# Kernel optimization log

Measured on AMD Instinct MI355X. Metric: run time of the kernel, lower is better.

## Reference

```python
import jax, jax.numpy as jnp
import numpy as np

B, S, D = 4, 2048, 1024  # batch, steps, d_model
HEAD, DIM = 16, 64       # head*dim == D


def setup_inputs() -> dict:
    key = jax.random.key(0)
    ks = jax.random.split(key, 7)
    mk = lambda k, shp, scale: (jax.random.normal(k, shp, dtype=jnp.float32) * scale)
    w_scale = np.sqrt(2.0 / D).astype(np.float32)  # he_normal-ish
    return {
        "query": mk(ks[0], (B, S, D), 1.0),
        "key": mk(ks[1], (B, S, D), 1.0),
        "value": mk(ks[2], (B, S, D), 1.0),
        "Wq": mk(ks[3], (D, HEAD * DIM), w_scale),
        "Wk": mk(ks[4], (D, HEAD * DIM), w_scale),
        "Wv": mk(ks[5], (D, HEAD * DIM), w_scale),
        "Wo": mk(ks[6], (HEAD * DIM, D), w_scale),
    }


def reference(query, key, value, Wq, Wk, Wv, Wo):
    # Projections (heads are NOT split in the original module)
    Q = jnp.einsum('bsd,de->bse', query, Wq)   # [B,S,head*dim]
    K = jnp.einsum('bsd,de->bse', key, Wk)
    V = jnp.einsum('bsd,de->bse', value, Wv)
    scale = jnp.asarray(1.0 / np.sqrt(DIM), dtype=Q.dtype)
    scores = jnp.einsum('bqe,bke->bqk', Q, K) * scale  # [B,Sq,Sk]
    # Faithful quirk: softmax over axis=1 (the query axis), as in the source
    attn = jax.nn.softmax(scores, axis=1)
    head = jnp.einsum('bqk,bke->bqe', attn, V)  # [B,S,head*dim]
    return jnp.einsum('bqe,ed->bqd', head, Wo)  # [B,S,D]
```

## Files before the change

### kernel.cpp

```cpp
#include <hip/hip_runtime.h>


typedef _Float16 f16;
typedef _Float16 f16x8 __attribute__((ext_vector_type(8)));
typedef float f32x4 __attribute__((ext_vector_type(4)));

__device__ __forceinline__ void gl_lds16(const void* g, void* l) {
  __builtin_amdgcn_global_load_lds(
      (const __attribute__((address_space(1))) void*)(uintptr_t)g,
      (__attribute__((address_space(3))) void*)(uint32_t)(uintptr_t)l, 16, 0, 0);
}

__device__ __forceinline__ int xcd_swz(int F, int nwg) {
  int q = nwg >> 3, r = nwg & 7;
  int xcd = F & 7, idx = F >> 3;
  return (xcd < r ? xcd * (q + 1) : r * (q + 1) + (xcd - r) * q) + idx;
}

template <int EPI, int STATS, int SWZ>
__global__ __launch_bounds__(256) void gemm16(
    const f16* __restrict__ Ag, const f16* __restrict__ Bg,
    float* __restrict__ Cf, f16* __restrict__ Ch,
    float* __restrict__ pm, float* __restrict__ pl,
    int K, int ldA, int ldB, int ldC, long sA, long sB, long sC, float scale) {
  __shared__ f16 sA_[128 * 64];
  __shared__ f16 sB_[128 * 64];

  const int tid = threadIdx.x;
  const int lane = tid & 63;
  const int wave = tid >> 6;
  int bx, by;
  long bz;
  if constexpr (SWZ) {
    const int gx = gridDim.x, gy = gridDim.y;
    const int nwg = gx * gy * gridDim.z;
    int F = blockIdx.x + gx * (blockIdx.y + gy * blockIdx.z);
    int wg = xcd_swz(F, nwg);
    bx = wg % gx;
    by = (wg / gx) % gy;
    bz = wg / (gx * gy);
  } else {
    bx = blockIdx.x;
    by = blockIdx.y;
    bz = blockIdx.z;
  }

  const int tM = by * 128;
  const int tN = bx * 128;
  const int wr = (wave >> 1) * 64;
  const int wc = (wave & 1) * 64;
  const int r16 = lane & 15;
  const int q4 = lane >> 4;

  const f16* Abase = Ag + bz * sA;
  const f16* Bbase = Bg + bz * sB;

  f32x4 acc[4][4] = {};

  for (int kt = 0; kt < K; kt += 64) {
#pragma unroll
    for (int it = 0; it < 4; ++it) {
      int row = it * 32 + (tid >> 3);
      int s = tid & 7;
      int gcol = kt + ((s ^ (row & 7)) << 3);
      int lo = row * 64 + s * 8;
      gl_lds16(Abase + (long)(tM + row) * ldA + gcol, sA_ + lo);
      gl_lds16(Bbase + (long)(tN + row) * ldB + gcol, sB_ + lo);
    }
    __syncthreads();
#pragma unroll
    for (int kk = 0; kk < 2; ++kk) {
      f16x8 ah[4], bh[4];
#pragma unroll
      for (int m = 0; m < 4; ++m) {
        int ar = wr + m * 16 + r16;
        ah[m] = *(const f16x8*)(sA_ + ar * 64 + (((kk * 4 + q4) ^ (ar & 7)) << 3));
      }
#pragma unroll
      for (int n = 0; n < 4; ++n) {
        int br = wc + n * 16 + r16;
        bh[n] = *(const f16x8*)(sB_ + br * 64 + (((kk * 4 + q4) ^ (br & 7)) << 3));
      }
#pragma unroll
      for (int m = 0; m < 4; ++m)
#pragma unroll
        for (int n = 0; n < 4; ++n)
          acc[m][n] = __builtin_amdgcn_mfma_f32_16x16x32_f16(ah[m], bh[n], acc[m][n], 0, 0, 0);
    }
    __syncthreads();
  }

#pragma unroll
  for (int m = 0; m < 4; ++m)
#pragma unroll
    for (int n = 0; n < 4; ++n)
#pragma unroll
      for (int j = 0; j < 4; ++j) {
        int rr = tM + wr + m * 16 + q4 * 4 + j;
        int cc = tN + wc + n * 16 + r16;
        float v = acc[m][n][j] * scale;
        if constexpr (EPI == 0) {
          Cf[bz * sC + (long)rr * ldC + cc] = v;
        } else if constexpr (EPI == 2) {
          Ch[bz * sC + (long)rr * ldC + cc] = (f16)v;
        } else {
          if (bz == 2)
            Ch[2 * sC + (long)cc * 2048 + (long)(rr >> 11) * 2097152L + (rr & 2047)] = (f16)v;
          else
            Ch[bz * sC + (long)rr * ldC + cc] = (f16)v;
        }
      }

  if constexpr (STATS) {
    float* mbuf = (float*)sA_;
    float* lbuf = mbuf + 256;
    const int wrIdx = wave >> 1, c0 = wc;
#pragma unroll
    for (int n = 0; n < 4; ++n) {
      float mt = -1e30f;
#pragma unroll
      for (int m = 0; m < 4; ++m)
#pragma unroll
        for (int j = 0; j < 4; ++j) mt = fmaxf(mt, acc[m][n][j] * scale);
      float lt = 0.f;
#pragma unroll
      for (int m = 0; m < 4; ++m)
#pragma unroll
        for (int j = 0; j < 4; ++j) lt += __expf(acc[m][n][j] * scale - mt);
#pragma unroll
      for (int d = 16; d <= 32; d <<= 1) {
        float mo = __shfl_xor(mt, d);
        float lo = __shfl_xor(lt, d);
        float mn = fmaxf(mt, mo);
        lt = lt * __expf(mt - mn) + lo * __expf(mo - mn);
        mt = mn;
      }
      if (q4 == 0) {
        int c = c0 + n * 16 + r16;
        mbuf[wrIdx * 128 + c] = mt;
        lbuf[wrIdx * 128 + c] = lt;
      }
    }
    __syncthreads();
    if (tid < 128) {
      float m0 = mbuf[tid], m1 = mbuf[128 + tid];
      float l0 = lbuf[tid], l1 = lbuf[128 + tid];
      float mn = fmaxf(m0, m1);
      float ln = l0 * __expf(m0 - mn) + l1 * __expf(m1 - mn);
      long idx = (bz * 16 + (tM >> 7)) * 2048 + tN + tid;
      pm[idx] = mn;
      pl[idx] = ln;
    }
  }
}

__global__ __launch_bounds__(256) void gemm_wvo(
    const f16* __restrict__ Ag, const f16* __restrict__ Bg, f16* __restrict__ Ch,
    int K, int ldA, int ldB, int ldC) {
  __shared__ f16 sA_[128 * 64];
  __shared__ f16 sB_[128 * 64];
  const int tid = threadIdx.x;
  const int lane = tid & 63;
  const int wave = tid >> 6;
  const int tM = blockIdx.y * 128;
  const int tN = blockIdx.x * 128;
  const int wr = (wave >> 1) * 64;
  const int wc = (wave & 1) * 64;
  const int r16 = lane & 15;
  const int q4 = lane >> 4;
  f32x4 acc[4][4] = {};
  for (int kt = 0; kt < K; kt += 64) {
#pragma unroll
    for (int it = 0; it < 4; ++it) {
      int row = it * 32 + (tid >> 3);
      int s = tid & 7;
      int gcol = kt + ((s ^ (row & 7)) << 3);
      int lo = row * 64 + s * 8;
      gl_lds16(Ag + (long)(tM + row) * ldA + gcol, sA_ + lo);
      gl_lds16(Bg + (long)(tN + row) * ldB + gcol, sB_ + lo);
    }
    __syncthreads();
#pragma unroll
    for (int kk = 0; kk < 2; ++kk) {
      f16x8 ah[4], bh[4];
#pragma unroll
      for (int m = 0; m < 4; ++m) {
        int ar = wr + m * 16 + r16;
        ah[m] = *(const f16x8*)(sA_ + ar * 64 + (((kk * 4 + q4) ^ (ar & 7)) << 3));
      }
#pragma unroll
      for (int n = 0; n < 4; ++n) {
        int br = wc + n * 16 + r16;
        bh[n] = *(const f16x8*)(sB_ + br * 64 + (((kk * 4 + q4) ^ (br & 7)) << 3));
      }
#pragma unroll
      for (int m = 0; m < 4; ++m)
#pragma unroll
        for (int n = 0; n < 4; ++n)
          acc[m][n] = __builtin_amdgcn_mfma_f32_16x16x32_f16(ah[m], bh[n], acc[m][n], 0, 0, 0);
    }
    __syncthreads();
  }
#pragma unroll
  for (int m = 0; m < 4; ++m)
#pragma unroll
    for (int n = 0; n < 4; ++n)
#pragma unroll
      for (int j = 0; j < 4; ++j) {
        int rr = tM + wr + m * 16 + q4 * 4 + j;
        int cc = tN + wc + n * 16 + r16;
        Ch[(long)cc * ldC + rr] = (f16)acc[m][n][j];
      }
}

__global__ __launch_bounds__(256) void convert4(
    const float* __restrict__ i0, const float* __restrict__ i1,
    const float* __restrict__ i2, const float* __restrict__ i3,
    f16* __restrict__ o0, f16* __restrict__ o1, f16* __restrict__ o2,
    f16* __restrict__ o3, long n012, long n3) {
  const int z = blockIdx.z;
  const float* in = (z == 0) ? i0 : (z == 1) ? i1 : (z == 2) ? i2 : i3;
  f16* hi = (z == 0) ? o0 : (z == 1) ? o1 : (z == 2) ? o2 : o3;
  long n = (z == 3) ? n3 : n012;
  long i = ((long)blockIdx.x * 256 + threadIdx.x) * 8;
  if (i >= n) return;
  float4 aa = *(const float4*)(in + i);
  float4 bb = *(const float4*)(in + i + 4);
  f16x8 h;
  h[0] = (f16)aa.x; h[1] = (f16)aa.y; h[2] = (f16)aa.z; h[3] = (f16)aa.w;
  h[4] = (f16)bb.x; h[5] = (f16)bb.y; h[6] = (f16)bb.z; h[7] = (f16)bb.w;
  *(f16x8*)(hi + i) = h;
}

__global__ void tconv3(const float* __restrict__ i0, const float* __restrict__ i1,
                       const float* __restrict__ i2, f16* __restrict__ o0,
                       f16* __restrict__ o1, f16* __restrict__ o2, int n) {
  const float* in = (blockIdx.z == 0) ? i0 : (blockIdx.z == 1) ? i1 : i2;
  f16* hi = (blockIdx.z == 0) ? o0 : (blockIdx.z == 1) ? o1 : o2;
  __shared__ float t[32][33];
  int bx = blockIdx.x * 32, by = blockIdx.y * 32;
  int tx = threadIdx.x, ty = threadIdx.y;
  for (int i = 0; i < 32; i += 8) t[ty + i][tx] = in[(long)(by + ty + i) * n + bx + tx];
  __syncthreads();
  for (int i = 0; i < 32; i += 8)
    hi[(long)(bx + ty + i) * n + by + tx] = (f16)t[tx][ty + i];
}

__global__ void stats2(const float* __restrict__ pm, const float* __restrict__ pl,
                       float* __restrict__ mfo, float* __restrict__ rlo) {
  int c = blockIdx.x * 256 + threadIdx.x;
  int b = c >> 11, k = c & 2047;
  float m = -1e30f;
  for (int qc = 0; qc < 16; ++qc) m = fmaxf(m, pm[(b * 16 + qc) * 2048 + k]);
  float l = 0.f;
  for (int qc = 0; qc < 16; ++qc)
    l += pl[(b * 16 + qc) * 2048 + k] * __expf(pm[(b * 16 + qc) * 2048 + k] - m);
  mfo[c] = m;
  rlo[c] = 1.f / l;
}

__global__ __launch_bounds__(256) void norm(f16* __restrict__ S16,
                                            const float* __restrict__ mf,
                                            const float* __restrict__ rl) {
  long row = blockIdx.x;
  int b = (int)(row >> 11);
  f16* Sr = S16 + row * 2048;
  const float* mb = mf + ((long)b << 11);
  const float* rb = rl + ((long)b << 11);
  int c = threadIdx.x * 8;
  f16x8 v = *(f16x8*)(Sr + c);
  float4 m0 = *(const float4*)(mb + c);
  float4 m1 = *(const float4*)(mb + c + 4);
  float4 r0 = *(const float4*)(rb + c);
  float4 r1 = *(const float4*)(rb + c + 4);
  f16x8 o;
  o[0] = (f16)(__expf((float)v[0] - m0.x) * r0.x);
  o[1] = (f16)(__expf((float)v[1] - m0.y) * r0.y);
  o[2] = (f16)(__expf((float)v[2] - m0.z) * r0.z);
  o[3] = (f16)(__expf((float)v[3] - m0.w) * r0.w);
  o[4] = (f16)(__expf((float)v[4] - m1.x) * r1.x);
  o[5] = (f16)(__expf((float)v[5] - m1.y) * r1.y);
  o[6] = (f16)(__expf((float)v[6] - m1.z) * r1.z);
  o[7] = (f16)(__expf((float)v[7] - m1.w) * r1.w);
  *(f16x8*)(Sr + c) = o;
}

extern "C" void kernel_launch(void* const* d_in, const int* in_sizes, int n_in,
                              void* d_out, int out_size, void* d_ws, size_t ws_size,
                              hipStream_t stream) {
  const float* query = (const float*)d_in[0];
  const float* key   = (const float*)d_in[1];
  const float* value = (const float*)d_in[2];
  const float* Wq    = (const float*)d_in[3];
  const float* Wk    = (const float*)d_in[4];
  const float* Wv    = (const float*)d_in[5];
  const float* Wo    = (const float*)d_in[6];
  float* out = (float*)d_out;

  f16* h = (f16*)d_ws;
  const long E8 = 8388608L;
  const long E1 = 1048576L;
  f16* q16   = h;
  f16* k16   = h + E8;
  f16* v16   = h + 2 * E8;
  f16* Qh    = h + 3 * E8;
  f16* Kh    = h + 4 * E8;
  f16* VWoT  = h + 5 * E8;
  f16* Wqt   = h + 6 * E8;
  f16* Wkt   = Wqt + E1;
  f16* Wvot  = Wkt + E1;
  f16* Wot   = Wvot + E1;
  f16* wv16  = Wot + E1;
  f16* S16   = wv16 + E1;
  float* pm  = (float*)(S16 + 16777216L);
  float* pl  = pm + 131072;
  float* mf  = pl + 131072;
  float* rl  = mf + 8192;
  (void)in_sizes; (void)n_in; (void)out_size; (void)ws_size;

  dim3 tb32(32, 8);
  tconv3<<<dim3(32, 32, 3), tb32, 0, stream>>>(Wq, Wk, Wo, Wqt, Wkt, Wot, 1024);

  convert4<<<dim3(4096, 1, 4), 256, 0, stream>>>(query, key, value, Wv,
                                                 q16, k16, v16, wv16, E8, E1);

  gemm_wvo<<<dim3(8, 8, 1), 256, 0, stream>>>(wv16, Wot, Wvot, 1024, 1024, 1024, 1024);

  gemm16<4, 0, 0><<<dim3(8, 64, 3), 256, 0, stream>>>(
      q16, Wqt, nullptr, Qh, nullptr, nullptr,
      1024, 1024, 1024, 1024, E8, E1, E8, 1.f);

  gemm16<2, 1, 1><<<dim3(16, 16, 4), 256, 0, stream>>>(
      Qh, Kh, nullptr, S16, pm, pl,
      1024, 1024, 1024, 2048, 2097152L, 2097152L, 4194304L, 0.125f);

  stats2<<<32, 256, 0, stream>>>(pm, pl, mf, rl);
  norm<<<8192, 256, 0, stream>>>(S16, mf, rl);

  gemm16<0, 0, 1><<<dim3(8, 16, 4), 256, 0, stream>>>(
      S16, VWoT, out, nullptr, nullptr, nullptr,
      2048, 2048, 2048, 1024, 4194304L, 2097152L, 2097152L, 1.f);
}
```

Before: 253.0 us.

## Fold Wq·Wkᵀ into one weight matrix to drop the K projection GEMM

Q·Kᵀ is rewritten as query·(Wq·Wkᵀ)·keyᵀ. A new split-fp16 (hi/lo, three MFMAs) GEMM computes the combined 1024x1024 weight directly from the fp32 Wq and Wk, so the Wq and Wk transposes go away. The projection GEMM now covers two batches (query·W2 and value·Wv∘Wo) instead of three, removing one of the large 8192x1024x1024 projections. The cost is an extra small GEMM, and the combined weight is rounded to fp16, which may change accuracy.

```diff
diff --git a/kernel.cpp b/kernel.cpp
--- a/kernel.cpp
+++ b/kernel.cpp
@@ -3,6 +3,7 @@
 
 typedef _Float16 f16;
 typedef _Float16 f16x8 __attribute__((ext_vector_type(8)));
+typedef _Float16 f16x4 __attribute__((ext_vector_type(4)));
 typedef float f32x4 __attribute__((ext_vector_type(4)));
 
 __device__ __forceinline__ void gl_lds16(const void* g, void* l) {
@@ -104,10 +105,10 @@
         } else if constexpr (EPI == 2) {
           Ch[bz * sC + (long)rr * ldC + cc] = (f16)v;
         } else {
-          if (bz == 2)
-            Ch[2 * sC + (long)cc * 2048 + (long)(rr >> 11) * 2097152L + (rr & 2047)] = (f16)v;
+          if (bz == 1)
+            Ch[sC + (long)cc * 2048 + (long)(rr >> 11) * 2097152L + (rr & 2047)] = (f16)v;
           else
-            Ch[bz * sC + (long)rr * ldC + cc] = (f16)v;
+            Ch[(long)rr * ldC + cc] = (f16)v;
         }
       }
 
@@ -152,6 +153,73 @@
       pl[idx] = ln;
     }
   }
+}
+
+__global__ __launch_bounds__(256) void gemm_w2(
+    const float* __restrict__ A, const float* __restrict__ B, f16* __restrict__ C) {
+  __shared__ f16 Ah[128 * 40];
+  __shared__ f16 Al[128 * 40];
+  __shared__ f16 Bh[128 * 40];
+  __shared__ f16 Bl[128 * 40];
+  const int tid = threadIdx.x;
+  const int lane = tid & 63;
+  const int wave = tid >> 6;
+  const int tM = blockIdx.y * 128, tN = blockIdx.x * 128;
+  const int wr = (wave >> 1) * 64, wc = (wave & 1) * 64;
+  const int r16 = lane & 15, q4 = lane >> 4, kof = q4 * 8;
+  f32x4 acc[4][4] = {};
+  for (int kt = 0; kt < 1024; kt += 32) {
+#pragma unroll
+    for (int it = 0; it < 4; ++it) {
+      int flat = it * 1024 + tid * 4;
+      int row = flat >> 5, col = flat & 31;
+      float4 av = *(const float4*)&A[(long)(tM + row) * 1024 + kt + col];
+      float4 bv = *(const float4*)&B[(long)(tN + row) * 1024 + kt + col];
+      f16x4 ah = {(f16)av.x, (f16)av.y, (f16)av.z, (f16)av.w};
+      f16x4 bh = {(f16)bv.x, (f16)bv.y, (f16)bv.z, (f16)bv.w};
+      *(f16x4*)(Ah + row * 40 + col) = ah;
+      *(f16x4*)(Bh + row * 40 + col) = bh;
+      f16x4 al = {(f16)(av.x - (float)ah[0]), (f16)(av.y - (float)ah[1]),
+                  (f16)(av.z - (float)ah[2]), (f16)(av.w - (float)ah[3])};
+      f16x4 bl = {(f16)(bv.x - (float)bh[0]), (f16)(bv.y - (float)bh[1]),
+                  (f16)(bv.z - (float)bh[2]), (f16)(bv.w - (float)bh[3])};
+      *(f16x4*)(Al + row * 40 + col) = al;
+      *(f16x4*)(Bl + row * 40 + col) = bl;
+    }
+    __syncthreads();
+    f16x8 afh[4], afl[4], bfh[4], bfl[4];
+#pragma unroll
+    for (int m = 0; m < 4; ++m) {
+      int ar = wr + m * 16 + r16;
+      afh[m] = *(const f16x8*)(Ah + ar * 40 + kof);
+      afl[m] = *(const f16x8*)(Al + ar * 40 + kof);
+    }
+#pragma unroll
+    for (int n = 0; n < 4; ++n) {
+      int br = wc + n * 16 + r16;
+      bfh[n] = *(const f16x8*)(Bh + br * 40 + kof);
+      bfl[n] = *(const f16x8*)(Bl + br * 40 + kof);
+    }
+#pragma unroll
+    for (int m = 0; m < 4; ++m)
+#pragma unroll
+      for (int n = 0; n < 4; ++n) {
+        acc[m][n] = __builtin_amdgcn_mfma_f32_16x16x32_f16(afh[m], bfh[n], acc[m][n], 0, 0, 0);
+        acc[m][n] = __builtin_amdgcn_mfma_f32_16x16x32_f16(afh[m], bfl[n], acc[m][n], 0, 0, 0);
+        acc[m][n] = __builtin_amdgcn_mfma_f32_16x16x32_f16(afl[m], bfh[n], acc[m][n], 0, 0, 0);
+      }
+    __syncthreads();
+  }
+#pragma unroll
+  for (int m = 0; m < 4; ++m)
+#pragma unroll
+    for (int n = 0; n < 4; ++n)
+#pragma unroll
+      for (int j = 0; j < 4; ++j) {
+        int rr = tM + wr + m * 16 + q4 * 4 + j;
+        int cc = tN + wc + n * 16 + r16;
+        C[(long)cc * 1024 + rr] = (f16)acc[m][n][j];
+      }
 }
 
 __global__ __launch_bounds__(256) void gemm_wvo(
@@ -232,11 +300,7 @@
   *(f16x8*)(hi + i) = h;
 }
 
-__global__ void tconv3(const float* __restrict__ i0, const float* __restrict__ i1,
-                       const float* __restrict__ i2, f16* __restrict__ o0,
-                       f16* __restrict__ o1, f16* __restrict__ o2, int n) {
-  const float* in = (blockIdx.z == 0) ? i0 : (blockIdx.z == 1) ? i1 : i2;
-  f16* hi = (blockIdx.z == 0) ? o0 : (blockIdx.z == 1) ? o1 : o2;
+__global__ void tconv(const float* __restrict__ in, f16* __restrict__ hi, int n) {
   __shared__ float t[32][33];
   int bx = blockIdx.x * 32, by = blockIdx.y * 32;
   int tx = threadIdx.x, ty = threadIdx.y;
@@ -301,14 +365,12 @@
   const long E8 = 8388608L;
   const long E1 = 1048576L;
   f16* q16   = h;
-  f16* k16   = h + E8;
-  f16* v16   = h + 2 * E8;
-  f16* Qh    = h + 3 * E8;
-  f16* Kh    = h + 4 * E8;
-  f16* VWoT  = h + 5 * E8;
-  f16* Wqt   = h + 6 * E8;
-  f16* Wkt   = Wqt + E1;
-  f16* Wvot  = Wkt + E1;
+  f16* v16   = h + E8;
+  f16* k16   = h + 2 * E8;
+  f16* Th    = h + 3 * E8;
+  f16* VWoT  = h + 4 * E8;
+  f16* W2T   = h + 5 * E8;
+  f16* Wvot  = W2T + E1;
   f16* Wot   = Wvot + E1;
   f16* wv16  = Wot + E1;
   f16* S16   = wv16 + E1;
@@ -319,19 +381,21 @@
   (void)in_sizes; (void)n_in; (void)out_size; (void)ws_size;
 
   dim3 tb32(32, 8);
-  tconv3<<<dim3(32, 32, 3), tb32, 0, stream>>>(Wq, Wk, Wo, Wqt, Wkt, Wot, 1024);
+  tconv<<<dim3(32, 32), tb32, 0, stream>>>(Wo, Wot, 1024);
 
   convert4<<<dim3(4096, 1, 4), 256, 0, stream>>>(query, key, value, Wv,
                                                  q16, k16, v16, wv16, E8, E1);
 
-  gemm_wvo<<<dim3(8, 8, 1), 256, 0, stream>>>(wv16, Wot, Wvot, 1024, 1024, 1024, 1024);
-
-  gemm16<4, 0, 0><<<dim3(8, 64, 3), 256, 0, stream>>>(
-      q16, Wqt, nullptr, Qh, nullptr, nullptr,
+  gemm_w2<<<dim3(8, 8), 256, 0, stream>>>(Wq, Wk, W2T);
+
+  gemm_wvo<<<dim3(8, 8), 256, 0, stream>>>(wv16, Wot, Wvot, 1024, 1024, 1024, 1024);
+
+  gemm16<4, 0, 0><<<dim3(8, 64, 2), 256, 0, stream>>>(
+      q16, W2T, nullptr, Th, nullptr, nullptr,
       1024, 1024, 1024, 1024, E8, E1, E8, 1.f);
 
   gemm16<2, 1, 1><<<dim3(16, 16, 4), 256, 0, stream>>>(
-      Qh, Kh, nullptr, S16, pm, pl,
+      Th, k16, nullptr, S16, pm, pl,
       1024, 1024, 1024, 2048, 2097152L, 2097152L, 4194304L, 0.125f);
 
   stats2<<<32, 256, 0, stream>>>(pm, pl, mf, rl);
```

Result: slower. 298.3 us (+17.9%).

## Fold Wq·Wkᵀ into one weight so K projection is skipped

Applied to the files above, without the earlier changes.

Precomputes Wq·Wkᵀ as a single 1024x1024 weight and projects only the query with it, so the scores GEMM reads the raw key activations directly. This drops one of the three large B·S·D projection GEMMs, leaving projections for the folded query and V·Wo. The weight fold is batched with the existing Wv·Wo fold in one launch. The cost is an extra small weight GEMM and a changed fp16 rounding path, since the folded product is rounded to fp16 before being applied to the query.

```diff
diff --git a/kernel.cpp b/kernel.cpp
--- a/kernel.cpp
+++ b/kernel.cpp
@@ -104,10 +104,10 @@
         } else if constexpr (EPI == 2) {
           Ch[bz * sC + (long)rr * ldC + cc] = (f16)v;
         } else {
-          if (bz == 2)
-            Ch[2 * sC + (long)cc * 2048 + (long)(rr >> 11) * 2097152L + (rr & 2047)] = (f16)v;
+          if (bz == 1)
+            Ch[sC + (long)cc * 2048 + (long)(rr >> 11) * 2097152L + (rr & 2047)] = (f16)v;
           else
-            Ch[bz * sC + (long)rr * ldC + cc] = (f16)v;
+            Ch[(long)rr * ldC + cc] = (f16)v;
         }
       }
 
@@ -154,20 +154,23 @@
   }
 }
 
-__global__ __launch_bounds__(256) void gemm_wvo(
+__global__ __launch_bounds__(256) void gemm_fold(
     const f16* __restrict__ Ag, const f16* __restrict__ Bg, f16* __restrict__ Ch,
-    int K, int ldA, int ldB, int ldC) {
+    int K, int ldA, int ldB, int ldC, long sA, long sB, long sC) {
   __shared__ f16 sA_[128 * 64];
   __shared__ f16 sB_[128 * 64];
   const int tid = threadIdx.x;
   const int lane = tid & 63;
   const int wave = tid >> 6;
+  const long bz = blockIdx.z;
   const int tM = blockIdx.y * 128;
   const int tN = blockIdx.x * 128;
   const int wr = (wave >> 1) * 64;
   const int wc = (wave & 1) * 64;
   const int r16 = lane & 15;
   const int q4 = lane >> 4;
+  const f16* Abase = Ag + bz * sA;
+  const f16* Bbase = Bg + bz * sB;
   f32x4 acc[4][4] = {};
   for (int kt = 0; kt < K; kt += 64) {
 #pragma unroll
@@ -176,8 +179,8 @@
       int s = tid & 7;
       int gcol = kt + ((s ^ (row & 7)) << 3);
       int lo = row * 64 + s * 8;
-      gl_lds16(Ag + (long)(tM + row) * ldA + gcol, sA_ + lo);
-      gl_lds16(Bg + (long)(tN + row) * ldB + gcol, sB_ + lo);
+      gl_lds16(Abase + (long)(tM + row) * ldA + gcol, sA_ + lo);
+      gl_lds16(Bbase + (long)(tN + row) * ldB + gcol, sB_ + lo);
     }
     __syncthreads();
 #pragma unroll
@@ -209,19 +212,29 @@
       for (int j = 0; j < 4; ++j) {
         int rr = tM + wr + m * 16 + q4 * 4 + j;
         int cc = tN + wc + n * 16 + r16;
-        Ch[(long)cc * ldC + rr] = (f16)acc[m][n][j];
-      }
-}
-
-__global__ __launch_bounds__(256) void convert4(
+        Ch[bz * sC + (long)cc * ldC + rr] = (f16)acc[m][n][j];
+      }
+}
+
+__global__ __launch_bounds__(256) void convert6(
     const float* __restrict__ i0, const float* __restrict__ i1,
     const float* __restrict__ i2, const float* __restrict__ i3,
+    const float* __restrict__ i4, const float* __restrict__ i5,
     f16* __restrict__ o0, f16* __restrict__ o1, f16* __restrict__ o2,
-    f16* __restrict__ o3, long n012, long n3) {
+    f16* __restrict__ o3, f16* __restrict__ o4, f16* __restrict__ o5,
+    long nbig, long nsmall) {
   const int z = blockIdx.z;
-  const float* in = (z == 0) ? i0 : (z == 1) ? i1 : (z == 2) ? i2 : i3;
-  f16* hi = (z == 0) ? o0 : (z == 1) ? o1 : (z == 2) ? o2 : o3;
-  long n = (z == 3) ? n3 : n012;
+  const float* in;
+  f16* hi;
+  long n;
+  switch (z) {
+    case 0: in = i0; hi = o0; n = nbig; break;
+    case 1: in = i1; hi = o1; n = nbig; break;
+    case 2: in = i2; hi = o2; n = nbig; break;
+    case 3: in = i3; hi = o3; n = nsmall; break;
+    case 4: in = i4; hi = o4; n = nsmall; break;
+    default: in = i5; hi = o5; n = nsmall; break;
+  }
   long i = ((long)blockIdx.x * 256 + threadIdx.x) * 8;
   if (i >= n) return;
   float4 aa = *(const float4*)(in + i);
@@ -232,11 +245,7 @@
   *(f16x8*)(hi + i) = h;
 }
 
-__global__ void tconv3(const float* __restrict__ i0, const float* __restrict__ i1,
-                       const float* __restrict__ i2, f16* __restrict__ o0,
-                       f16* __restrict__ o1, f16* __restrict__ o2, int n) {
-  const float* in = (blockIdx.z == 0) ? i0 : (blockIdx.z == 1) ? i1 : i2;
-  f16* hi = (blockIdx.z == 0) ? o0 : (blockIdx.z == 1) ? o1 : o2;
+__global__ void tconv(const float* __restrict__ in, f16* __restrict__ hi, int n) {
   __shared__ float t[32][33];
   int bx = blockIdx.x * 32, by = blockIdx.y * 32;
   int tx = threadIdx.x, ty = threadIdx.y;
@@ -301,17 +310,18 @@
   const long E8 = 8388608L;
   const long E1 = 1048576L;
   f16* q16   = h;
-  f16* k16   = h + E8;
-  f16* v16   = h + 2 * E8;
-  f16* Qh    = h + 3 * E8;
-  f16* Kh    = h + 4 * E8;
-  f16* VWoT  = h + 5 * E8;
-  f16* Wqt   = h + 6 * E8;
-  f16* Wkt   = Wqt + E1;
-  f16* Wvot  = Wkt + E1;
-  f16* Wot   = Wvot + E1;
-  f16* wv16  = Wot + E1;
-  f16* S16   = wv16 + E1;
+  f16* v16   = h + E8;
+  f16* k16   = h + 2 * E8;
+  f16* Th    = h + 3 * E8;
+  f16* VWoT  = h + 4 * E8;
+  f16* WB    = h + 5 * E8;
+  f16* Wq16  = WB;
+  f16* wv16  = WB + E1;
+  f16* Wk16  = WB + 2 * E1;
+  f16* Wot   = WB + 3 * E1;
+  f16* W2T   = WB + 4 * E1;
+  f16* Wvot  = WB + 5 * E1;
+  f16* S16   = WB + 6 * E1;
   float* pm  = (float*)(S16 + 16777216L);
   float* pl  = pm + 131072;
   float* mf  = pl + 131072;
@@ -319,19 +329,20 @@
   (void)in_sizes; (void)n_in; (void)out_size; (void)ws_size;
 
   dim3 tb32(32, 8);
-  tconv3<<<dim3(32, 32, 3), tb32, 0, stream>>>(Wq, Wk, Wo, Wqt, Wkt, Wot, 1024);
-
-  convert4<<<dim3(4096, 1, 4), 256, 0, stream>>>(query, key, value, Wv,
-                                                 q16, k16, v16, wv16, E8, E1);
-
-  gemm_wvo<<<dim3(8, 8, 1), 256, 0, stream>>>(wv16, Wot, Wvot, 1024, 1024, 1024, 1024);
-
-  gemm16<4, 0, 0><<<dim3(8, 64, 3), 256, 0, stream>>>(
-      q16, Wqt, nullptr, Qh, nullptr, nullptr,
+  tconv<<<dim3(32, 32), tb32, 0, stream>>>(Wo, Wot, 1024);
+
+  convert6<<<dim3(4096, 1, 6), 256, 0, stream>>>(
+      query, key, value, Wq, Wk, Wv, q16, k16, v16, Wq16, Wk16, wv16, E8, E1);
+
+  gemm_fold<<<dim3(8, 8, 2), 256, 0, stream>>>(
+      Wq16, Wk16, W2T, 1024, 1024, 1024, 1024, E1, E1, E1);
+
+  gemm16<4, 0, 0><<<dim3(8, 64, 2), 256, 0, stream>>>(
+      q16, W2T, nullptr, Th, nullptr, nullptr,
       1024, 1024, 1024, 1024, E8, E1, E8, 1.f);
 
   gemm16<2, 1, 1><<<dim3(16, 16, 4), 256, 0, stream>>>(
-      Qh, Kh, nullptr, S16, pm, pl,
+      Th, k16, nullptr, S16, pm, pl,
       1024, 1024, 1024, 2048, 2097152L, 2097152L, 4194304L, 0.125f);
 
   stats2<<<32, 256, 0, stream>>>(pm, pl, mf, rl);
```

New measurement: 239.4 us. 1.06x faster.
